# Kernel optimization log

Hardware: AMD Instinct MI355X
Metric: run time of the kernel (lower is better)

The kernel has to match this reference:

```python
import jax, jax.numpy as jnp
import numpy as np

B, Q, D = 8, 128, 2048
H, HD = 16, 128           # num_heads, head_dim (D == H*HD)
CACHE = 3968              # tokens already in KV cache; CACHE+Q == max_seq_len


def setup_inputs() -> dict:
    key = jax.random.key(0)
    ks = jax.random.split(key, 6)
    x = jax.random.normal(ks[0], (B, Q, D), dtype=jnp.float32)
    k_cache = jax.random.normal(ks[1], (B, H, CACHE, HD), dtype=jnp.float32)
    v_cache = jax.random.normal(ks[2], (B, H, CACHE, HD), dtype=jnp.float32)
    Wqkv = jax.random.normal(ks[3], (D, 3 * D), dtype=jnp.float32) * 0.02
    Wproj = jax.random.normal(ks[4], (D, D), dtype=jnp.float32) * 0.02
    bproj = jnp.zeros((D,), dtype=jnp.float32)
    return {"x": x, "k_cache": k_cache, "v_cache": v_cache,
            "Wqkv": Wqkv, "Wproj": Wproj, "bproj": bproj}


def reference(x, k_cache, v_cache, Wqkv, Wproj, bproj):
    # QKV projection (qkv_bias=False)
    qkv = x @ Wqkv                                   # [B, Q, 3D]
    qkv = qkv.reshape(B, Q, 3, H, HD)
    qkv = jnp.transpose(qkv, (2, 0, 3, 1, 4))        # [3, B, H, Q, HD]
    q, k_new, v_new = qkv[0], qkv[1], qkv[2]
    # KV-cache append (cache_pos + Q == max_seq_len, no roll)
    k_all = jnp.concatenate([k_cache, k_new], axis=2)  # [B, H, K, HD]
    v_all = jnp.concatenate([v_cache, v_new], axis=2)
    K = CACHE + Q
    scale = 1.0 / jnp.sqrt(jnp.float32(HD))
    scores = jnp.einsum('bhqd,bhkd->bhqk', q, k_all) * scale  # [B, H, Q, K]
    # Causal mask aligned to cache (bottom-right): query i sees keys j <= i + (K - Q)
    i = jnp.arange(Q)[:, None]
    j = jnp.arange(K)[None, :]
    mask = j > (i + (K - Q))
    scores = jnp.where(mask, jnp.float32(-jnp.inf), scores)
    attn = jax.nn.softmax(scores, axis=-1)
    out = jnp.einsum('bhqk,bhkd->bhqd', attn, v_all)   # [B, H, Q, HD]
    out = jnp.transpose(out, (0, 2, 1, 3)).reshape(B, Q, D)
    return out @ Wproj + bproj
```

## Files before the change

kernel.cpp:

```cpp
#include <hip/hip_runtime.h>

typedef unsigned int u32;
typedef unsigned short u16;
typedef short s16x8 __attribute__((ext_vector_type(8)));
typedef float f32x4 __attribute__((ext_vector_type(4)));

#define MFMA16(a,b,c) __builtin_amdgcn_mfma_f32_16x16x32_bf16((a),(b),(c),0,0,0)

#define Bb 8
#define Hh 16
#define Qq 128
#define HDd 128
#define Dd 2048
#define CACHE 3968
#define NSPLIT 8
#define SCALE 0.08838834764831845f

__device__ __forceinline__ u16 f2bf(float x){
  u32 u = __builtin_bit_cast(u32, x);
  u32 r = ((u >> 16) & 1u) + 0x7fffu;
  return (u16)((u + r) >> 16);
}
__device__ __forceinline__ float bf2f(u16 h){
  return __builtin_bit_cast(float, ((u32)h) << 16);
}
__device__ __forceinline__ u32 pk2(float a, float b){
  return (u32)f2bf(a) | ((u32)f2bf(b) << 16);
}
__device__ __forceinline__ float f4c(const float4& v, int j){
  return j==0 ? v.x : j==1 ? v.y : j==2 ? v.z : v.w;
}
__device__ __forceinline__ void gload_lds16(const void* g, void* l){
  __builtin_amdgcn_global_load_lds(
      (const __attribute__((address_space(1))) u32*)g,
      (__attribute__((address_space(3))) u32*)l, 16, 0, 0);
}

__global__ void k_cvt(const float* __restrict__ s, u16* __restrict__ d, int n4){
  int i = blockIdx.x * 256 + threadIdx.x;
  if (i < n4){
    float4 v = *(const float4*)(s + (size_t)i * 4);
    *(uint2*)(d + (size_t)i * 4) = make_uint2(pk2(v.x, v.y), pk2(v.z, v.w));
  }
}

__global__ void k_tcvt(const float* __restrict__ s, u16* __restrict__ d, int R, int C){
  __shared__ float t[32][33];
  int tx = threadIdx.x & 31, ty = threadIdx.x >> 5;
  int c0 = blockIdx.x * 32, r0 = blockIdx.y * 32;
#pragma unroll
  for (int i = 0; i < 4; i++)
    t[ty + i*8][tx] = s[(size_t)(r0 + ty + i*8) * C + c0 + tx];
  __syncthreads();
#pragma unroll
  for (int i = 0; i < 4; i++)
    d[(size_t)(c0 + ty + i*8) * R + r0 + tx] = f2bf(t[tx][ty + i*8]);
}

template<int MODE>
__global__ __launch_bounds__(256)
void k_gemm(const u16* __restrict__ A, const u16* __restrict__ Bt, int K, int N,
            u16* __restrict__ oq, u16* __restrict__ ok, u16* __restrict__ ov,
            float* __restrict__ of, const float* __restrict__ bias)
{
  const int m0 = blockIdx.y * 128, n0 = blockIdx.x * 128;
  const int tid = threadIdx.x;
  const int w = tid >> 6, l = tid & 63;
  const int lg = l >> 4, lr = l & 15;
  const int wr = w >> 1, wc = w & 1;

  __shared__ u16 As[2][128 * 32];
  __shared__ u16 Bs[2][128 * 32];

  f32x4 acc[4][4];
#pragma unroll
  for (int i = 0; i < 4; i++)
#pragma unroll
    for (int j = 0; j < 4; j++) acc[i][j] = f32x4{0.f, 0.f, 0.f, 0.f};

  const int nt = K >> 5;

  auto stage = [&](int buf, int t){
    const int k0 = t << 5;
#pragma unroll
    for (int i = 0; i < 2; i++){
      int flat = i * 256 + tid;
      int row = flat >> 2, kq = flat & 3;
      const u16* ga = A + (size_t)(m0 + row) * K + k0 + kq * 8;
      gload_lds16(ga, (char*)&As[buf][0] + (size_t)(i*256 + w*64) * 16);
      const u16* gb = Bt + (size_t)(n0 + row) * K + k0 + kq * 8;
      gload_lds16(gb, (char*)&Bs[buf][0] + (size_t)(i*256 + w*64) * 16);
    }
  };

  stage(0, 0);
  asm volatile("s_waitcnt vmcnt(0)" ::: "memory");
  __syncthreads();

  for (int t = 0; t < nt; ++t){
    const int buf = t & 1;
    if (t + 1 < nt) stage(buf ^ 1, t + 1);
    s16x8 af[4], bfr[4];
#pragma unroll
    for (int i = 0; i < 4; i++){
      int row = wr*64 + i*16 + lr;
      af[i] = *(const s16x8*)&As[buf][row*32 + lg*8];
    }
#pragma unroll
    for (int j = 0; j < 4; j++){
      int col = wc*64 + j*16 + lr;
      bfr[j] = *(const s16x8*)&Bs[buf][col*32 + lg*8];
    }
#pragma unroll
    for (int i = 0; i < 4; i++)
#pragma unroll
      for (int j = 0; j < 4; j++)
        acc[i][j] = MFMA16(af[i], bfr[j], acc[i][j]);
    asm volatile("s_waitcnt vmcnt(0)" ::: "memory");
    __syncthreads();
  }

#pragma unroll
  for (int i = 0; i < 4; i++){
#pragma unroll
    for (int j = 0; j < 4; j++){
#pragma unroll
      for (int r = 0; r < 4; r++){
        int m = m0 + wr*64 + i*16 + lg*4 + r;
        int n = n0 + wc*64 + j*16 + lr;
        float v = acc[i][j][r];
        if (MODE == 0){
          int which = n >> 11;
          int h = (n >> 7) & 15, hd = n & 127;
          int b = m >> 7, qi = m & 127;
          size_t idx = (((size_t)(b * Hh + h)) * Qq + qi) * HDd + hd;
          if (which == 0)      oq[idx] = f2bf(v * SCALE);
          else if (which == 1) ok[idx] = f2bf(v);
          else                 ov[idx] = f2bf(v);
        } else {
          of[(size_t)m * N + n] = v + bias[n];
        }
      }
    }
  }
}

__global__ __launch_bounds__(512)
void k_attn(const float* __restrict__ kc, const float* __restrict__ vc,
            const u16* __restrict__ qw, const u16* __restrict__ knw,
            const u16* __restrict__ vnw, float* __restrict__ opart,
            float2* __restrict__ ml)
{
  const int bh = blockIdx.x >> 3;
  const int sg = blockIdx.x & 7;
  const int tid = threadIdx.x;
  const int w = tid >> 6, l = tid & 63;
  const int lg = l >> 4, lr = l & 15;

  __shared__ u16 Ks[64 * 136];
  __shared__ u32 Vts[128 * 32];
  __shared__ u16 Pl[8 * 16 * 72];

  s16x8 qf[4];
  {
    const u16* qp = qw + (((size_t)bh * Qq + w*16 + lr) * HDd);
#pragma unroll
    for (int kk = 0; kk < 4; kk++) qf[kk] = *(const s16x8*)(qp + kk*32 + lg*8);
  }

  f32x4 acc[8];
#pragma unroll
  for (int i = 0; i < 8; i++) acc[i] = f32x4{0.f, 0.f, 0.f, 0.f};
  float mrow[4], lsum[4];
#pragma unroll
  for (int r = 0; r < 4; r++){ mrow[r] = -__builtin_inff(); lsum[r] = 0.f; }

  const float* kbase = kc + (size_t)bh * CACHE * HDd;
  const float* vbase = vc + (size_t)bh * CACHE * HDd;
  const u16* knb = knw + (size_t)bh * Qq * HDd;
  const u16* vnb = vnw + (size_t)bh * Qq * HDd;

  const int rv = tid & 15, c4v = tid >> 4;

  float4 kreg[4], vreg[4];

  auto loadc = [&](int c){
    if (c < 62){
#pragma unroll
      for (int i = 0; i < 4; i++){
        int flat = tid + i*512;
        int row = flat >> 5, c4 = flat & 31;
        kreg[i] = *(const float4*)(kbase + ((size_t)(c*64 + row)) * HDd + c4*4);
      }
#pragma unroll
      for (int a = 0; a < 4; a++)
        vreg[a] = *(const float4*)(vbase + ((size_t)(c*64 + rv + a*16)) * HDd + c4v*4);
    } else {
#pragma unroll
      for (int i = 0; i < 4; i++){
        int flat = tid + i*512;
        int row = flat >> 5, c4 = flat & 31;
        ushort4 u = *(const ushort4*)(knb + ((size_t)(c*64 + row - CACHE)) * HDd + c4*4);
        kreg[i] = make_float4(bf2f(u.x), bf2f(u.y), bf2f(u.z), bf2f(u.w));
      }
#pragma unroll
      for (int a = 0; a < 4; a++){
        ushort4 u = *(const ushort4*)(vnb + ((size_t)(c*64 + rv + a*16 - CACHE)) * HDd + c4v*4);
        vreg[a] = make_float4(bf2f(u.x), bf2f(u.y), bf2f(u.z), bf2f(u.w));
      }
    }
  };

  loadc(sg * 8);

  for (int cl = 0; cl < 8; ++cl){
    const int c = sg * 8 + cl;
#pragma unroll
    for (int i = 0; i < 4; i++){
      int flat = tid + i*512;
      int row = flat >> 5, c4 = flat & 31;
      *(uint2*)&Ks[row*136 + c4*4] =
          make_uint2(pk2(kreg[i].x, kreg[i].y), pk2(kreg[i].z, kreg[i].w));
    }
#pragma unroll
    for (int j = 0; j < 4; j++){
      int col = c4v*4 + j;
      int x2 = (col & 7) << 2;
      Vts[col*32 + (rv ^ x2)]        = pk2(f4c(vreg[0], j), f4c(vreg[1], j));
      Vts[col*32 + ((rv + 16) ^ x2)] = pk2(f4c(vreg[2], j), f4c(vreg[3], j));
    }
    __syncthreads();
    if (cl + 1 < 8) loadc(c + 1);

    f32x4 s[4];
#pragma unroll
    for (int t = 0; t < 4; t++){
      s[t] = f32x4{0.f, 0.f, 0.f, 0.f};
      const u16* kp = &Ks[(t*16 + lr) * 136];
#pragma unroll
      for (int kk = 0; kk < 4; kk++){
        s16x8 kf = *(const s16x8*)(kp + kk*32 + lg*8);
        s[t] = MFMA16(qf[kk], kf, s[t]);
      }
    }
    if (c >= 62){
      int jn = c*64 - CACHE;
#pragma unroll
      for (int t = 0; t < 4; t++){
        int kn = jn + t*16 + lr;
#pragma unroll
        for (int r = 0; r < 4; r++){
          int qi = w*16 + lg*4 + r;
          if (kn > qi) s[t][r] = -__builtin_inff();
        }
      }
    }
    float corr[4];
#pragma unroll
    for (int r = 0; r < 4; r++){
      float v = fmaxf(fmaxf(s[0][r], s[1][r]), fmaxf(s[2][r], s[3][r]));
      v = fmaxf(v, __shfl_xor(v, 1));
      v = fmaxf(v, __shfl_xor(v, 2));
      v = fmaxf(v, __shfl_xor(v, 4));
      v = fmaxf(v, __shfl_xor(v, 8));
      float mn = fmaxf(mrow[r], v);
      corr[r] = __expf(mrow[r] - mn);
      mrow[r] = mn;
    }
    float ps[4] = {0.f, 0.f, 0.f, 0.f};
#pragma unroll
    for (int t = 0; t < 4; t++)
#pragma unroll
      for (int r = 0; r < 4; r++){
        float p = __expf(s[t][r] - mrow[r]);
        s[t][r] = p;
        ps[r] += p;
      }
#pragma unroll
    for (int r = 0; r < 4; r++){
      float v = ps[r];
      v += __shfl_xor(v, 1);
      v += __shfl_xor(v, 2);
      v += __shfl_xor(v, 4);
      v += __shfl_xor(v, 8);
      lsum[r] = lsum[r] * corr[r] + v;
    }
#pragma unroll
    for (int i = 0; i < 8; i++)
#pragma unroll
      for (int r = 0; r < 4; r++) acc[i][r] *= corr[r];

    u16* pw = &Pl[w * 16 * 72];
#pragma unroll
    for (int t = 0; t < 4; t++){
      int pos = ((t >> 1) << 5) + 2*lr + (t & 1);
#pragma unroll
      for (int r = 0; r < 4; r++)
        pw[(lg*4 + r) * 72 + pos] = f2bf(s[t][r]);
    }
    s16x8 pf[2];
#pragma unroll
    for (int kk = 0; kk < 2; kk++)
      pf[kk] = *(const s16x8*)(pw + lr*72 + kk*32 + lg*8);

#pragma unroll
    for (int t = 0; t < 8; t++){
      int col = t*16 + lr;
      const u32* vp = &Vts[col * 32];
#pragma unroll
      for (int kk = 0; kk < 2; kk++){
        s16x8 vf = *(const s16x8*)(vp + ((16*kk + 4*lg) ^ ((col & 7) << 2)));
        acc[t] = MFMA16(pf[kk], vf, acc[t]);
      }
    }
    __syncthreads();
  }

  float* pbase = opart + (size_t)blockIdx.x * (Qq * HDd);
#pragma unroll
  for (int t = 0; t < 8; t++){
#pragma unroll
    for (int r = 0; r < 4; r++){
      int qi = w*16 + lg*4 + r;
      pbase[(size_t)qi * HDd + t*16 + lr] = acc[t][r];
    }
  }
  if (lr == 0){
#pragma unroll
    for (int r = 0; r < 4; r++){
      int qi = w*16 + lg*4 + r;
      ml[(size_t)blockIdx.x * Qq + qi] = make_float2(mrow[r], lsum[r]);
    }
  }
}

__global__ __launch_bounds__(256)
void k_comb(const float* __restrict__ opart, const float2* __restrict__ ml,
            u16* __restrict__ ao)
{
  const int bh = blockIdx.x >> 2;
  const int q0 = (blockIdx.x & 3) * 32;
  const int tid = threadIdx.x;

  __shared__ float wgt[32][NSPLIT];
  __shared__ float Ls[32];

  {
    int row = tid >> 3, s = tid & 7;
    float2 v = ml[((size_t)(bh * NSPLIT + s)) * Qq + q0 + row];
    float m = v.x;
    m = fmaxf(m, __shfl_xor(m, 1));
    m = fmaxf(m, __shfl_xor(m, 2));
    m = fmaxf(m, __shfl_xor(m, 4));
    float e = __expf(v.x - m);
    float el = e * v.y;
    el += __shfl_xor(el, 1);
    el += __shfl_xor(el, 2);
    el += __shfl_xor(el, 4);
    wgt[row][s] = e;
    if (s == 0) Ls[row] = el;
  }
  __syncthreads();

  const int cp = tid & 63;
  const int r4 = tid >> 6;
  const int b = bh >> 4, h = bh & 15;
#pragma unroll
  for (int rr = 0; rr < 8; rr++){
    int row = r4 + rr*4;
    float2 a = make_float2(0.f, 0.f);
    const float* pb = opart + ((size_t)(bh * NSPLIT)) * (Qq * HDd)
                            + (size_t)(q0 + row) * HDd + cp*2;
#pragma unroll
    for (int s = 0; s < NSPLIT; s++){
      float2 p = *(const float2*)(pb + (size_t)s * (Qq * HDd));
      float wv = wgt[row][s];
      a.x += wv * p.x;
      a.y += wv * p.y;
    }
    float inv = 1.0f / Ls[row];
    u16* dst = ao + ((size_t)b * Qq + q0 + row) * Dd + h * HDd + cp*2;
    *(u32*)dst = pk2(a.x * inv, a.y * inv);
  }
}

extern "C" void kernel_launch(void* const* d_in, const int* in_sizes, int n_in,
                              void* d_out, int out_size, void* d_ws, size_t ws_size,
                              hipStream_t stream)
{
  const float* x     = (const float*)d_in[0];
  const float* kc    = (const float*)d_in[1];
  const float* vc    = (const float*)d_in[2];
  const float* wqkv  = (const float*)d_in[3];
  const float* wproj = (const float*)d_in[4];
  const float* bproj = (const float*)d_in[5];
  float* out = (float*)d_out;

  char* ws = (char*)d_ws;
  u16* xb  = (u16*)(ws);
  u16* wtq = (u16*)(ws + ((size_t)4  << 20));
  u16* wtp = (u16*)(ws + ((size_t)28 << 20));
  u16* qw  = (u16*)(ws + ((size_t)36 << 20));
  u16* knw = (u16*)(ws + ((size_t)40 << 20));
  u16* vnw = (u16*)(ws + ((size_t)44 << 20));
  u16* aow = (u16*)(ws + ((size_t)48 << 20));
  float* opart = (float*)(ws + ((size_t)52 << 20));
  float2* mlw  = (float2*)(ws + ((size_t)116 << 20));

  k_cvt<<<2048, 256, 0, stream>>>(x, xb, (1024 * 2048) / 4);
  k_tcvt<<<dim3(192, 64), 256, 0, stream>>>(wqkv, wtq, 2048, 6144);
  k_tcvt<<<dim3(64, 64), 256, 0, stream>>>(wproj, wtp, 2048, 2048);
  k_gemm<0><<<dim3(48, 8), 256, 0, stream>>>(xb, wtq, 2048, 6144,
                                             qw, knw, vnw, nullptr, nullptr);
  k_attn<<<Bb * Hh * NSPLIT, 512, 0, stream>>>(kc, vc, qw, knw, vnw, opart, mlw);
  k_comb<<<Bb * Hh * 4, 256, 0, stream>>>(opart, mlw, aow);
  k_gemm<1><<<dim3(16, 8), 256, 0, stream>>>(aow, wtp, 2048, 2048,
                                             nullptr, nullptr, nullptr, out, bproj);
}
```

Baseline: 304.9 us.

## Halve attention block to 256 threads, each wave handling two query tiles

The attention kernel now runs 4 waves per block instead of 8, and each wave computes two 16-row query tiles. Each K and V fragment read from LDS then feeds two MFMAs, which halves LDS fragment traffic per FLOP. Each thread also loads twice as many K/V elements per chunk. The cost is roughly double the per-thread register footprint (accumulators, prefetch registers), with launch_bounds(256,2) asking the compiler to fit two blocks per CU.

Result: slower. 408.6 us (+34.0%).

```diff
diff --git a/kernel.cpp b/kernel.cpp
--- a/kernel.cpp
+++ b/kernel.cpp
@@ -145,7 +145,7 @@
   }
 }
 
-__global__ __launch_bounds__(512)
+__global__ __launch_bounds__(256, 2)
 void k_attn(const float* __restrict__ kc, const float* __restrict__ vc,
             const u16* __restrict__ qw, const u16* __restrict__ knw,
             const u16* __restrict__ vnw, float* __restrict__ opart,
@@ -159,55 +159,66 @@
 
   __shared__ u16 Ks[64 * 136];
   __shared__ u32 Vts[128 * 32];
-  __shared__ u16 Pl[8 * 16 * 72];
-
-  s16x8 qf[4];
-  {
-    const u16* qp = qw + (((size_t)bh * Qq + w*16 + lr) * HDd);
-#pragma unroll
-    for (int kk = 0; kk < 4; kk++) qf[kk] = *(const s16x8*)(qp + kk*32 + lg*8);
-  }
-
-  f32x4 acc[8];
-#pragma unroll
-  for (int i = 0; i < 8; i++) acc[i] = f32x4{0.f, 0.f, 0.f, 0.f};
-  float mrow[4], lsum[4];
-#pragma unroll
-  for (int r = 0; r < 4; r++){ mrow[r] = -__builtin_inff(); lsum[r] = 0.f; }
+  __shared__ u16 Pl[4 * 32 * 72];
+
+  s16x8 qf[2][4];
+#pragma unroll
+  for (int u = 0; u < 2; u++){
+    const u16* qp = qw + (((size_t)bh * Qq + w*32 + u*16 + lr) * HDd);
+#pragma unroll
+    for (int kk = 0; kk < 4; kk++) qf[u][kk] = *(const s16x8*)(qp + kk*32 + lg*8);
+  }
+
+  f32x4 acc[2][8];
+#pragma unroll
+  for (int u = 0; u < 2; u++)
+#pragma unroll
+    for (int i = 0; i < 8; i++) acc[u][i] = f32x4{0.f, 0.f, 0.f, 0.f};
+  float mrow[2][4], lsum[2][4];
+#pragma unroll
+  for (int u = 0; u < 2; u++)
+#pragma unroll
+    for (int r = 0; r < 4; r++){ mrow[u][r] = -__builtin_inff(); lsum[u][r] = 0.f; }
 
   const float* kbase = kc + (size_t)bh * CACHE * HDd;
   const float* vbase = vc + (size_t)bh * CACHE * HDd;
   const u16* knb = knw + (size_t)bh * Qq * HDd;
   const u16* vnb = vnw + (size_t)bh * Qq * HDd;
 
-  const int rv = tid & 15, c4v = tid >> 4;
-
-  float4 kreg[4], vreg[4];
+  const int rv = tid & 15, c4v2 = tid >> 4;
+
+  float4 kreg[8], vreg[8];
 
   auto loadc = [&](int c){
     if (c < 62){
 #pragma unroll
-      for (int i = 0; i < 4; i++){
-        int flat = tid + i*512;
+      for (int i = 0; i < 8; i++){
+        int flat = tid + i*256;
         int row = flat >> 5, c4 = flat & 31;
         kreg[i] = *(const float4*)(kbase + ((size_t)(c*64 + row)) * HDd + c4*4);
       }
 #pragma unroll
-      for (int a = 0; a < 4; a++)
-        vreg[a] = *(const float4*)(vbase + ((size_t)(c*64 + rv + a*16)) * HDd + c4v*4);
+      for (int hh = 0; hh < 2; hh++)
+#pragma unroll
+        for (int a = 0; a < 4; a++)
+          vreg[hh*4+a] = *(const float4*)(vbase + ((size_t)(c*64 + rv + a*16)) * HDd
+                                          + (c4v2 + hh*16)*4);
     } else {
 #pragma unroll
-      for (int i = 0; i < 4; i++){
-        int flat = tid + i*512;
+      for (int i = 0; i < 8; i++){
+        int flat = tid + i*256;
         int row = flat >> 5, c4 = flat & 31;
         ushort4 u = *(const ushort4*)(knb + ((size_t)(c*64 + row - CACHE)) * HDd + c4*4);
         kreg[i] = make_float4(bf2f(u.x), bf2f(u.y), bf2f(u.z), bf2f(u.w));
       }
 #pragma unroll
-      for (int a = 0; a < 4; a++){
-        ushort4 u = *(const ushort4*)(vnb + ((size_t)(c*64 + rv + a*16 - CACHE)) * HDd + c4v*4);
-        vreg[a] = make_float4(bf2f(u.x), bf2f(u.y), bf2f(u.z), bf2f(u.w));
-      }
+      for (int hh = 0; hh < 2; hh++)
+#pragma unroll
+        for (int a = 0; a < 4; a++){
+          ushort4 u = *(const ushort4*)(vnb + ((size_t)(c*64 + rv + a*16 - CACHE)) * HDd
+                                        + (c4v2 + hh*16)*4);
+          vreg[hh*4+a] = make_float4(bf2f(u.x), bf2f(u.y), bf2f(u.z), bf2f(u.w));
+        }
     }
   };
 
@@ -216,92 +227,105 @@
   for (int cl = 0; cl < 8; ++cl){
     const int c = sg * 8 + cl;
 #pragma unroll
-    for (int i = 0; i < 4; i++){
-      int flat = tid + i*512;
+    for (int i = 0; i < 8; i++){
+      int flat = tid + i*256;
       int row = flat >> 5, c4 = flat & 31;
       *(uint2*)&Ks[row*136 + c4*4] =
           make_uint2(pk2(kreg[i].x, kreg[i].y), pk2(kreg[i].z, kreg[i].w));
     }
 #pragma unroll
-    for (int j = 0; j < 4; j++){
-      int col = c4v*4 + j;
-      int x2 = (col & 7) << 2;
-      Vts[col*32 + (rv ^ x2)]        = pk2(f4c(vreg[0], j), f4c(vreg[1], j));
-      Vts[col*32 + ((rv + 16) ^ x2)] = pk2(f4c(vreg[2], j), f4c(vreg[3], j));
-    }
+    for (int hh = 0; hh < 2; hh++)
+#pragma unroll
+      for (int j = 0; j < 4; j++){
+        int col = (c4v2 + hh*16)*4 + j;
+        int x2 = (col & 7) << 2;
+        Vts[col*32 + (rv ^ x2)]        = pk2(f4c(vreg[hh*4+0], j), f4c(vreg[hh*4+1], j));
+        Vts[col*32 + ((rv + 16) ^ x2)] = pk2(f4c(vreg[hh*4+2], j), f4c(vreg[hh*4+3], j));
+      }
     __syncthreads();
     if (cl + 1 < 8) loadc(c + 1);
 
-    f32x4 s[4];
+    f32x4 s[2][4];
+#pragma unroll
+    for (int u = 0; u < 2; u++)
+#pragma unroll
+      for (int t = 0; t < 4; t++) s[u][t] = f32x4{0.f, 0.f, 0.f, 0.f};
 #pragma unroll
     for (int t = 0; t < 4; t++){
-      s[t] = f32x4{0.f, 0.f, 0.f, 0.f};
       const u16* kp = &Ks[(t*16 + lr) * 136];
 #pragma unroll
       for (int kk = 0; kk < 4; kk++){
         s16x8 kf = *(const s16x8*)(kp + kk*32 + lg*8);
-        s[t] = MFMA16(qf[kk], kf, s[t]);
+        s[0][t] = MFMA16(qf[0][kk], kf, s[0][t]);
+        s[1][t] = MFMA16(qf[1][kk], kf, s[1][t]);
       }
     }
     if (c >= 62){
       int jn = c*64 - CACHE;
 #pragma unroll
+      for (int u = 0; u < 2; u++)
+#pragma unroll
+        for (int t = 0; t < 4; t++){
+          int kn = jn + t*16 + lr;
+#pragma unroll
+          for (int r = 0; r < 4; r++){
+            int qi = w*32 + u*16 + lg*4 + r;
+            if (kn > qi) s[u][t][r] = -__builtin_inff();
+          }
+        }
+    }
+#pragma unroll
+    for (int u = 0; u < 2; u++){
+      float corr[4];
+#pragma unroll
+      for (int r = 0; r < 4; r++){
+        float v = fmaxf(fmaxf(s[u][0][r], s[u][1][r]), fmaxf(s[u][2][r], s[u][3][r]));
+        v = fmaxf(v, __shfl_xor(v, 1));
+        v = fmaxf(v, __shfl_xor(v, 2));
+        v = fmaxf(v, __shfl_xor(v, 4));
+        v = fmaxf(v, __shfl_xor(v, 8));
+        float mn = fmaxf(mrow[u][r], v);
+        corr[r] = __expf(mrow[u][r] - mn);
+        mrow[u][r] = mn;
+      }
+      float ps[4] = {0.f, 0.f, 0.f, 0.f};
+#pragma unroll
+      for (int t = 0; t < 4; t++)
+#pragma unroll
+        for (int r = 0; r < 4; r++){
+          float p = __expf(s[u][t][r] - mrow[u][r]);
+          s[u][t][r] = p;
+          ps[r] += p;
+        }
+#pragma unroll
+      for (int r = 0; r < 4; r++){
+        float v = ps[r];
+        v += __shfl_xor(v, 1);
+        v += __shfl_xor(v, 2);
+        v += __shfl_xor(v, 4);
+        v += __shfl_xor(v, 8);
+        lsum[u][r] = lsum[u][r] * corr[r] + v;
+      }
+#pragma unroll
+      for (int i = 0; i < 8; i++)
+#pragma unroll
+        for (int r = 0; r < 4; r++) acc[u][i][r] *= corr[r];
+
+      u16* pw = &Pl[(w*32 + u*16) * 72];
+#pragma unroll
       for (int t = 0; t < 4; t++){
-        int kn = jn + t*16 + lr;
-#pragma unroll
-        for (int r = 0; r < 4; r++){
-          int qi = w*16 + lg*4 + r;
-          if (kn > qi) s[t][r] = -__builtin_inff();
-        }
-      }
-    }
-    float corr[4];
-#pragma unroll
-    for (int r = 0; r < 4; r++){
-      float v = fmaxf(fmaxf(s[0][r], s[1][r]), fmaxf(s[2][r], s[3][r]));
-      v = fmaxf(v, __shfl_xor(v, 1));
-      v = fmaxf(v, __shfl_xor(v, 2));
-      v = fmaxf(v, __shfl_xor(v, 4));
-      v = fmaxf(v, __shfl_xor(v, 8));
-      float mn = fmaxf(mrow[r], v);
-      corr[r] = __expf(mrow[r] - mn);
-      mrow[r] = mn;
-    }
-    float ps[4] = {0.f, 0.f, 0.f, 0.f};
-#pragma unroll
-    for (int t = 0; t < 4; t++)
-#pragma unroll
-      for (int r = 0; r < 4; r++){
-        float p = __expf(s[t][r] - mrow[r]);
-        s[t][r] = p;
-        ps[r] += p;
-      }
-#pragma unroll
-    for (int r = 0; r < 4; r++){
-      float v = ps[r];
-      v += __shfl_xor(v, 1);
-      v += __shfl_xor(v, 2);
-      v += __shfl_xor(v, 4);
-      v += __shfl_xor(v, 8);
-      lsum[r] = lsum[r] * corr[r] + v;
-    }
-#pragma unroll
-    for (int i = 0; i < 8; i++)
-#pragma unroll
-      for (int r = 0; r < 4; r++) acc[i][r] *= corr[r];
-
-    u16* pw = &Pl[w * 16 * 72];
-#pragma unroll
-    for (int t = 0; t < 4; t++){
-      int pos = ((t >> 1) << 5) + 2*lr + (t & 1);
-#pragma unroll
-      for (int r = 0; r < 4; r++)
-        pw[(lg*4 + r) * 72 + pos] = f2bf(s[t][r]);
-    }
-    s16x8 pf[2];
-#pragma unroll
-    for (int kk = 0; kk < 2; kk++)
-      pf[kk] = *(const s16x8*)(pw + lr*72 + kk*32 + lg*8);
+        int pos = ((t >> 1) << 5) + 2*lr + (t & 1);
+#pragma unroll
+        for (int r = 0; r < 4; r++)
+          pw[(lg*4 + r) * 72 + pos] = f2bf(s[u][t][r]);
+      }
+    }
+    s16x8 pfr[2][2];
+#pragma unroll
+    for (int u = 0; u < 2; u++)
+#pragma unroll
+      for (int kk = 0; kk < 2; kk++)
+        pfr[u][kk] = *(const s16x8*)(&Pl[(w*32 + u*16 + lr) * 72] + kk*32 + lg*8);
 
 #pragma unroll
     for (int t = 0; t < 8; t++){
@@ -310,7 +334,8 @@
 #pragma unroll
       for (int kk = 0; kk < 2; kk++){
         s16x8 vf = *(const s16x8*)(vp + ((16*kk + 4*lg) ^ ((col & 7) << 2)));
-        acc[t] = MFMA16(pf[kk], vf, acc[t]);
+        acc[0][t] = MFMA16(pfr[0][kk], vf, acc[0][t]);
+        acc[1][t] = MFMA16(pfr[1][kk], vf, acc[1][t]);
       }
     }
     __syncthreads();
@@ -318,19 +343,24 @@
 
   float* pbase = opart + (size_t)blockIdx.x * (Qq * HDd);
 #pragma unroll
-  for (int t = 0; t < 8; t++){
-#pragma unroll
-    for (int r = 0; r < 4; r++){
-      int qi = w*16 + lg*4 + r;
-      pbase[(size_t)qi * HDd + t*16 + lr] = acc[t][r];
+  for (int u = 0; u < 2; u++){
+#pragma unroll
+    for (int t = 0; t < 8; t++){
+#pragma unroll
+      for (int r = 0; r < 4; r++){
+        int qi = w*32 + u*16 + lg*4 + r;
+        pbase[(size_t)qi * HDd + t*16 + lr] = acc[u][t][r];
+      }
     }
   }
   if (lr == 0){
 #pragma unroll
-    for (int r = 0; r < 4; r++){
-      int qi = w*16 + lg*4 + r;
-      ml[(size_t)blockIdx.x * Qq + qi] = make_float2(mrow[r], lsum[r]);
-    }
+    for (int u = 0; u < 2; u++)
+#pragma unroll
+      for (int r = 0; r < 4; r++){
+        int qi = w*32 + u*16 + lg*4 + r;
+        ml[(size_t)blockIdx.x * Qq + qi] = make_float2(mrow[u][r], lsum[u][r]);
+      }
   }
 }
 
@@ -412,7 +442,7 @@
   k_tcvt<<<dim3(64, 64), 256, 0, stream>>>(wproj, wtp, 2048, 2048);
   k_gemm<0><<<dim3(48, 8), 256, 0, stream>>>(xb, wtq, 2048, 6144,
                                              qw, knw, vnw, nullptr, nullptr);
-  k_attn<<<Bb * Hh * NSPLIT, 512, 0, stream>>>(kc, vc, qw, knw, vnw, opart, mlw);
+  k_attn<<<Bb * Hh * NSPLIT, 256, 0, stream>>>(kc, vc, qw, knw, vnw, opart, mlw);
   k_comb<<<Bb * Hh * 4, 256, 0, stream>>>(opart, mlw, aow);
   k_gemm<1><<<dim3(16, 8), 256, 0, stream>>>(aow, wtp, 2048, 2048,
                                              nullptr, nullptr, nullptr, out, bproj);
```
